# Kernel optimization log

Hardware: AMD Instinct MI355X
Metric: run time of the kernel (lower is better)

## Reference

```python
import jax, jax.numpy as jnp
import numpy as np

K, N, M = 65536, 4096, 64  # observations, basis centers, features


def setup_inputs() -> dict:
    key = jax.random.key(0)
    k1, k2, k3, k4 = jax.random.split(key, 4)
    x = jax.random.normal(k1, (K, M), dtype=jnp.float32)
    x_basis = jax.random.normal(k2, (N, M), dtype=jnp.float32)
    w = jax.random.normal(k3, (1, N), dtype=jnp.float32) / np.sqrt(N)
    b = jax.random.normal(k4, (1,), dtype=jnp.float32)
    return {"x": x, "x_basis": x_basis, "w": w, "b": b}


def reference(x, x_basis, w, b):
    # pairwise squared distances ||x_i - c_j||^2, [K, N]
    x2 = jnp.sum(x * x, axis=1, keepdims=True)          # [K, 1]
    c2 = jnp.sum(x_basis * x_basis, axis=1)             # [N]
    sq = x2 + c2[None, :] - 2.0 * (x @ x_basis.T)       # [K, N]
    phi = jnp.exp(-sq)                                  # gaussian RBF
    return jax.nn.sigmoid(phi @ w.T + b)                # [K, 1]
```

## Files before the change

kernel.cpp:

```cpp
#include <hip/hip_runtime.h>


#define KOBS 65536
#define NCENT 4096
#define MFEAT 64
#define NCHUNK 32

#define SCALE_A 2.8853900817779268f
#define QS      1.4426950408889634f
#define TSKIP   -60.0f

typedef __attribute__((ext_vector_type(4)))  float float4v;
typedef __attribute__((ext_vector_type(2)))  float float2v;
typedef __attribute__((ext_vector_type(16))) float float16v;
typedef __attribute__((ext_vector_type(8)))  int   int8v;

#if __has_builtin(__builtin_amdgcn_exp2f)
#define EXP2F(x) __builtin_amdgcn_exp2f(x)
#else
#define EXP2F(x) exp2f(x)
#endif

#define MFMA(A, B, C) __builtin_amdgcn_mfma_scale_f32_32x32x64_f8f6f4( \
    (A), (B), (C), 0, 0, 0, 0x7f7f7f7f, 0, 0x7f7f7f7f)

__global__ __launch_bounds__(256) void rbf_prep(
    const float* __restrict__ xb, const float* __restrict__ w,
    char* __restrict__ cb, float2v* __restrict__ hc2w) {
    const int bid = blockIdx.x;
    const int tid = threadIdx.x;
    if (bid < 128) {
        const int o      = bid * 256 + tid;
        const int col    = o >> 3;
        const int joct   = o & 7;
        const int c      = col >> 7;
        const int w4     = (col >> 5) & 3;
        const int lanelo = col & 31;
        const int l      = lanelo + (joct >> 2) * 32;
        const int j0     = (joct & 3) * 8;
        const float* src = xb + col * MFEAT + joct * 8;
        float4v v0 = *(const float4v*)(src);
        float4v v1 = *(const float4v*)(src + 4);
        int lo = __builtin_amdgcn_cvt_pk_fp8_f32(v0[0], v0[1], 0, false);
        lo     = __builtin_amdgcn_cvt_pk_fp8_f32(v0[2], v0[3], lo, true);
        int hi = __builtin_amdgcn_cvt_pk_fp8_f32(v1[0], v1[1], 0, false);
        hi     = __builtin_amdgcn_cvt_pk_fp8_f32(v1[2], v1[3], hi, true);
        unsigned long long pk = (unsigned long long)(unsigned)lo |
                                ((unsigned long long)(unsigned)hi << 32);
        *(unsigned long long*)(cb + (size_t)((c * 4 + w4) * 64 + l) * 32 + j0) = pk;
    } else {
        const int row  = (bid - 128) * 4 + (tid >> 6);
        const int lane = tid & 63;
        float v = xb[row * MFEAT + lane];
        float s = v * v;
        #pragma unroll
        for (int off = 32; off > 0; off >>= 1) s += __shfl_xor(s, off, 64);
        if (lane == 0) {
            float2v hw = {TSKIP + QS * s, w[row]};
            hc2w[row] = hw;
        }
    }
}

__global__ __launch_bounds__(512, 4) void rbf_main(
    const float* __restrict__ x, const char* __restrict__ cb,
    const float2v* __restrict__ hc2w, const float* __restrict__ bptr,
    float* __restrict__ out) {
    __shared__ float x2s[128];
    __shared__ float zl[128];

    const int tid  = threadIdx.x;
    const int wv   = tid >> 6;
    const int lane = tid & 63;
    const int ll   = lane & 31;
    const int lh   = lane >> 5;
    const int rt   = wv >> 2;
    const int wq   = wv & 3;
    const int bid  = (int)blockIdx.x;

    if (tid < 128) zl[tid] = 0.0f;

    const int r0e = bid * 128 + rt * 64;
    int8v af0, af1;
    #pragma unroll
    for (int t = 0; t < 2; ++t) {
        const float* xr = x + (size_t)(r0e + t * 32 + ll) * MFEAT + lh * 32;
        int8v a;
        float ss = 0.0f;
        #pragma unroll
        for (int rg = 0; rg < 8; ++rg) {
            float4v v = *(const float4v*)(xr + rg * 4);
            ss = fmaf(v[0], v[0], ss); ss = fmaf(v[1], v[1], ss);
            ss = fmaf(v[2], v[2], ss); ss = fmaf(v[3], v[3], ss);
            int pk = __builtin_amdgcn_cvt_pk_fp8_f32(
                SCALE_A * v[0], SCALE_A * v[1], 0, false);
            pk = __builtin_amdgcn_cvt_pk_fp8_f32(
                SCALE_A * v[2], SCALE_A * v[3], pk, true);
            a[rg] = pk;
        }
        ss += __shfl_xor(ss, 32, 64);
        if (t == 0) af0 = a; else af1 = a;
        if (wq == 0 && lh == 0) x2s[rt * 64 + t * 32 + ll] = ss;
    }
    __syncthreads();

    const int rb = 4 * lh;
    float16v p0, p1;
    #pragma unroll
    for (int i = 0; i < 16; ++i) {
        const int ri = rb + (i & 3) + 8 * (i >> 2);
        p0[i] = -QS * x2s[rt * 64 + ri];
        p1[i] = -QS * x2s[rt * 64 + 32 + ri];
    }

    const int zbase = rt * 64 + rb;
    const char*    cbb = cb + (size_t)(wq * 64 + lane) * 32;
    const float2v* hwp = hc2w + wq * 32 + ll;

    int8v   pb[2];
    float2v phw[2];

    #define LOADB(c, s) do {                                   \
        pb[s]  = *(const int8v*)(cbb + (size_t)(c) * 8192);    \
        phw[s] = hwp[(c) * 128];                               \
    } while (0)

    LOADB(0, 0);

    #pragma unroll 2
    for (int c = 0; c < NCHUNK; ++c) {
        const int cur = c & 1, nxt = cur ^ 1;
        if (c + 1 < NCHUNK) LOADB(c + 1, nxt);
        float16v a0 = MFMA(af0, pb[cur], p0);
        float16v a1 = MFMA(af1, pb[cur], p1);
        const float tq  = phw[cur].x;
        const float wv_ = phw[cur].y;
        #pragma unroll
        for (int t = 0; t < 2; ++t) {
            float16v av = t ? a1 : a0;
            float m0 = fmaxf(fmaxf(av[0],  av[1]),  av[2]);
            float m1 = fmaxf(fmaxf(av[3],  av[4]),  av[5]);
            float m2 = fmaxf(fmaxf(av[6],  av[7]),  av[8]);
            float m3 = fmaxf(fmaxf(av[9],  av[10]), av[11]);
            float m4 = fmaxf(fmaxf(av[12], av[13]), av[14]);
            float mx = fmaxf(fmaxf(fmaxf(m0, m1), m2),
                             fmaxf(fmaxf(m3, m4), av[15]));
            if (__any(mx > tq)) {
                if (mx > tq) {
                    const float q = TSKIP - tq;
                    #pragma unroll
                    for (int i = 0; i < 16; ++i)
                        atomicAdd(&zl[zbase + t * 32 + (i & 3) + 8 * (i >> 2)],
                                  wv_ * EXP2F(av[i] + q));
                }
            }
        }
    }
    #undef LOADB

    __syncthreads();
    if (tid < 128) {
        const float z = zl[tid] + bptr[0];
        out[bid * 128 + tid] = 1.0f / (1.0f + EXP2F(-QS * z));
    }
}

extern "C" void kernel_launch(void* const* d_in, const int* in_sizes, int n_in,
                              void* d_out, int out_size, void* d_ws, size_t ws_size,
                              hipStream_t stream) {
    const float* x  = (const float*)d_in[0];
    const float* xb = (const float*)d_in[1];
    const float* w  = (const float*)d_in[2];
    const float* b  = (const float*)d_in[3];
    float* out = (float*)d_out;

    char*    cb   = (char*)d_ws;
    float2v* hc2w = (float2v*)((char*)d_ws + NCENT * MFEAT);

    rbf_prep<<<128 + NCENT / 4, 256, 0, stream>>>(xb, w, cb, hc2w);
    rbf_main<<<KOBS / 128, 512, 0, stream>>>(x, cb, hc2w, b, out);
}
```

Baseline: 91.09 us.

## Triple-buffer center loads, pack threshold/weight as bf16 pair, merge skip test

Prefetch depth goes from two to three slots, with the chunk loop manually unrolled by three and the last two steps peeled, so B-fragment loads have more time to land before the MFMAs need them. The per-center threshold and weight are packed as two bf16 halves in one 32-bit word instead of a float2, halving that load. The two row-tile skip checks are merged into a single wave vote. The bf16 rounding of the threshold and weight loses precision, which can shift which terms are skipped and slightly change the output.

Result: faster. 88.23 us (-3.1%).

```diff
diff --git a/kernel.cpp b/kernel.cpp
--- a/kernel.cpp
+++ b/kernel.cpp
@@ -11,7 +11,6 @@
 #define TSKIP   -60.0f
 
 typedef __attribute__((ext_vector_type(4)))  float float4v;
-typedef __attribute__((ext_vector_type(2)))  float float2v;
 typedef __attribute__((ext_vector_type(16))) float float16v;
 typedef __attribute__((ext_vector_type(8)))  int   int8v;
 
@@ -21,12 +20,17 @@
 #define EXP2F(x) exp2f(x)
 #endif
 
+static __device__ inline unsigned f2bfu(float f) {
+    unsigned u = __float_as_uint(f);
+    return (u + 0x7fffu + ((u >> 16) & 1u)) >> 16;
+}
+
 #define MFMA(A, B, C) __builtin_amdgcn_mfma_scale_f32_32x32x64_f8f6f4( \
     (A), (B), (C), 0, 0, 0, 0x7f7f7f7f, 0, 0x7f7f7f7f)
 
 __global__ __launch_bounds__(256) void rbf_prep(
     const float* __restrict__ xb, const float* __restrict__ w,
-    char* __restrict__ cb, float2v* __restrict__ hc2w) {
+    char* __restrict__ cb, unsigned* __restrict__ hcw) {
     const int bid = blockIdx.x;
     const int tid = threadIdx.x;
     if (bid < 128) {
@@ -55,16 +59,14 @@
         float s = v * v;
         #pragma unroll
         for (int off = 32; off > 0; off >>= 1) s += __shfl_xor(s, off, 64);
-        if (lane == 0) {
-            float2v hw = {TSKIP + QS * s, w[row]};
-            hc2w[row] = hw;
-        }
+        if (lane == 0)
+            hcw[row] = (f2bfu(TSKIP + QS * s) << 16) | f2bfu(w[row]);
     }
 }
 
 __global__ __launch_bounds__(512, 4) void rbf_main(
     const float* __restrict__ x, const char* __restrict__ cb,
-    const float2v* __restrict__ hc2w, const float* __restrict__ bptr,
+    const unsigned* __restrict__ hcw, const float* __restrict__ bptr,
     float* __restrict__ out) {
     __shared__ float x2s[128];
     __shared__ float zl[128];
@@ -114,48 +116,68 @@
     }
 
     const int zbase = rt * 64 + rb;
-    const char*    cbb = cb + (size_t)(wq * 64 + lane) * 32;
-    const float2v* hwp = hc2w + wq * 32 + ll;
-
-    int8v   pb[2];
-    float2v phw[2];
-
-    #define LOADB(c, s) do {                                   \
-        pb[s]  = *(const int8v*)(cbb + (size_t)(c) * 8192);    \
-        phw[s] = hwp[(c) * 128];                               \
+    const unsigned cboff = (unsigned)(wq * 64 + lane) * 32u;
+    const unsigned moff  = (unsigned)(wq * 32 + ll);
+
+    int8v    pb[3];
+    unsigned mw[3];
+
+    #define LOADB(C, S) do {                                               \
+        pb[S] = *(const int8v*)(cb + cboff + (unsigned)(C) * 8192u);       \
+        mw[S] = hcw[moff + (unsigned)(C) * 128u];                          \
     } while (0)
 
+    #define STEP(C, SCUR, SPRE, DOLOAD) do {                               \
+        if (DOLOAD) LOADB((C) + 2, SPRE);                                  \
+        float16v a0 = MFMA(af0, pb[SCUR], p0);                             \
+        float16v a1 = MFMA(af1, pb[SCUR], p1);                             \
+        const unsigned mu = mw[SCUR];                                      \
+        const float tq  = __uint_as_float(mu & 0xffff0000u);               \
+        const float wv_ = __uint_as_float(mu << 16);                       \
+        float uA0 = fmaxf(fmaxf(a0[0],  a0[1]),  a0[2]);                   \
+        float uA1 = fmaxf(fmaxf(a0[3],  a0[4]),  a0[5]);                   \
+        float uA2 = fmaxf(fmaxf(a0[6],  a0[7]),  a0[8]);                   \
+        float uA3 = fmaxf(fmaxf(a0[9],  a0[10]), a0[11]);                  \
+        float uA4 = fmaxf(fmaxf(a0[12], a0[13]), a0[14]);                  \
+        float mA  = fmaxf(fmaxf(fmaxf(uA0, uA1), uA2),                     \
+                          fmaxf(fmaxf(uA3, uA4), a0[15]));                 \
+        float uB0 = fmaxf(fmaxf(a1[0],  a1[1]),  a1[2]);                   \
+        float uB1 = fmaxf(fmaxf(a1[3],  a1[4]),  a1[5]);                   \
+        float uB2 = fmaxf(fmaxf(a1[6],  a1[7]),  a1[8]);                   \
+        float uB3 = fmaxf(fmaxf(a1[9],  a1[10]), a1[11]);                  \
+        float uB4 = fmaxf(fmaxf(a1[12], a1[13]), a1[14]);                  \
+        float mB  = fmaxf(fmaxf(fmaxf(uB0, uB1), uB2),                     \
+                          fmaxf(fmaxf(uB3, uB4), a1[15]));                 \
+        if (__any(fmaxf(mA, mB) > tq)) {         \
+            const float q = TSKIP - tq;              \
+            if (mA > tq) {                                                 \
+                _Pragma("unroll")                                          \
+                for (int i_ = 0; i_ < 16; ++i_)                            \
+                    atomicAdd(&zl[zbase + (i_ & 3) + 8 * (i_ >> 2)],       \
+                              wv_ * EXP2F(a0[i_] + q));                    \
+            }                                                              \
+            if (mB > tq) {                                                 \
+                _Pragma("unroll")                                          \
+                for (int i_ = 0; i_ < 16; ++i_)                            \
+                    atomicAdd(&zl[zbase + 32 + (i_ & 3) + 8 * (i_ >> 2)],  \
+                              wv_ * EXP2F(a1[i_] + q));                    \
+            }                                                              \
+        }                                                                  \
+    } while (0)
+
     LOADB(0, 0);
-
-    #pragma unroll 2
-    for (int c = 0; c < NCHUNK; ++c) {
-        const int cur = c & 1, nxt = cur ^ 1;
-        if (c + 1 < NCHUNK) LOADB(c + 1, nxt);
-        float16v a0 = MFMA(af0, pb[cur], p0);
-        float16v a1 = MFMA(af1, pb[cur], p1);
-        const float tq  = phw[cur].x;
-        const float wv_ = phw[cur].y;
-        #pragma unroll
-        for (int t = 0; t < 2; ++t) {
-            float16v av = t ? a1 : a0;
-            float m0 = fmaxf(fmaxf(av[0],  av[1]),  av[2]);
-            float m1 = fmaxf(fmaxf(av[3],  av[4]),  av[5]);
-            float m2 = fmaxf(fmaxf(av[6],  av[7]),  av[8]);
-            float m3 = fmaxf(fmaxf(av[9],  av[10]), av[11]);
-            float m4 = fmaxf(fmaxf(av[12], av[13]), av[14]);
-            float mx = fmaxf(fmaxf(fmaxf(m0, m1), m2),
-                             fmaxf(fmaxf(m3, m4), av[15]));
-            if (__any(mx > tq)) {
-                if (mx > tq) {
-                    const float q = TSKIP - tq;
-                    #pragma unroll
-                    for (int i = 0; i < 16; ++i)
-                        atomicAdd(&zl[zbase + t * 32 + (i & 3) + 8 * (i >> 2)],
-                                  wv_ * EXP2F(av[i] + q));
-                }
-            }
-        }
-    }
+    LOADB(1, 1);
+
+    #pragma unroll 1
+    for (int c = 0; c < 30; c += 3) {
+        STEP(c,     0, 2, 1);
+        STEP(c + 1, 1, 0, 1);
+        STEP(c + 2, 2, 1, 1);
+    }
+    STEP(30, 0, 2, 0);
+    STEP(31, 1, 0, 0);
+
+    #undef STEP
     #undef LOADB
 
     __syncthreads();
@@ -174,9 +196,9 @@
     const float* b  = (const float*)d_in[3];
     float* out = (float*)d_out;
 
-    char*    cb   = (char*)d_ws;
-    float2v* hc2w = (float2v*)((char*)d_ws + NCENT * MFEAT);
-
-    rbf_prep<<<128 + NCENT / 4, 256, 0, stream>>>(xb, w, cb, hc2w);
-    rbf_main<<<KOBS / 128, 512, 0, stream>>>(x, cb, hc2w, b, out);
-}
+    char*     cb  = (char*)d_ws;
+    unsigned* hcw = (unsigned*)((char*)d_ws + NCENT * MFEAT);
+
+    rbf_prep<<<128 + NCENT / 4, 256, 0, stream>>>(xb, w, cb, hcw);
+    rbf_main<<<KOBS / 128, 512, 0, stream>>>(x, cb, hcw, b, out);
+}
```

## Stage basis chunks through double-buffered LDS and pack threshold/weight as bf16 pair

Applied to the files above, without the earlier changes.

Each wave used to load its fp8 basis fragment straight from global memory. Now the block cooperatively copies each 8KB chunk into a padded, double-buffered shared-memory tile and syncs once per chunk. This cuts redundant global and L2 traffic, since the two row-tile waves shared the same B data. The per-center threshold and weight are packed as two bf16 values in one 32-bit word, and the skip test is merged across both row tiles. The costs are a block-wide barrier every iteration, no loop unrolling, and reduced precision on the threshold and weight.

Measured after the change: 89.06 us. 1.02x faster.

```diff
diff --git a/kernel.cpp b/kernel.cpp
--- a/kernel.cpp
+++ b/kernel.cpp
@@ -10,10 +10,10 @@
 #define QS      1.4426950408889634f
 #define TSKIP   -60.0f
 
-typedef __attribute__((ext_vector_type(4)))  float float4v;
-typedef __attribute__((ext_vector_type(2)))  float float2v;
-typedef __attribute__((ext_vector_type(16))) float float16v;
-typedef __attribute__((ext_vector_type(8)))  int   int8v;
+typedef __attribute__((ext_vector_type(4)))  float    float4v;
+typedef __attribute__((ext_vector_type(16))) float    float16v;
+typedef __attribute__((ext_vector_type(8)))  int      int8v;
+typedef __attribute__((ext_vector_type(4)))  unsigned uint4v;
 
 #if __has_builtin(__builtin_amdgcn_exp2f)
 #define EXP2F(x) __builtin_amdgcn_exp2f(x)
@@ -21,12 +21,20 @@
 #define EXP2F(x) exp2f(x)
 #endif
 
+static __device__ inline unsigned f2bfu(float f) {
+    unsigned u = __float_as_uint(f);
+    return (u + 0x7fffu + ((u >> 16) & 1u)) >> 16;
+}
+
 #define MFMA(A, B, C) __builtin_amdgcn_mfma_scale_f32_32x32x64_f8f6f4( \
     (A), (B), (C), 0, 0, 0, 0x7f7f7f7f, 0, 0x7f7f7f7f)
 
+#define LROW(r) (((r) >> 2) * 144 + ((r) & 3) * 32)
+#define LBUFSZ  (64 * 144)
+
 __global__ __launch_bounds__(256) void rbf_prep(
     const float* __restrict__ xb, const float* __restrict__ w,
-    char* __restrict__ cb, float2v* __restrict__ hc2w) {
+    char* __restrict__ cb, unsigned* __restrict__ hcw) {
     const int bid = blockIdx.x;
     const int tid = threadIdx.x;
     if (bid < 128) {
@@ -55,19 +63,18 @@
         float s = v * v;
         #pragma unroll
         for (int off = 32; off > 0; off >>= 1) s += __shfl_xor(s, off, 64);
-        if (lane == 0) {
-            float2v hw = {TSKIP + QS * s, w[row]};
-            hc2w[row] = hw;
-        }
+        if (lane == 0)
+            hcw[row] = (f2bfu(TSKIP + QS * s) << 16) | f2bfu(w[row]);
     }
 }
 
 __global__ __launch_bounds__(512, 4) void rbf_main(
     const float* __restrict__ x, const char* __restrict__ cb,
-    const float2v* __restrict__ hc2w, const float* __restrict__ bptr,
+    const unsigned* __restrict__ hcw, const float* __restrict__ bptr,
     float* __restrict__ out) {
     __shared__ float x2s[128];
     __shared__ float zl[128];
+    __shared__ char  bs[2][LBUFSZ];
 
     const int tid  = threadIdx.x;
     const int wv   = tid >> 6;
@@ -102,6 +109,12 @@
         if (t == 0) af0 = a; else af1 = a;
         if (wq == 0 && lh == 0) x2s[rt * 64 + t * 32 + ll] = ss;
     }
+
+    const unsigned sdst = (unsigned)(LROW(tid >> 1) + (tid & 1) * 16);
+    uint4v stg = *(const uint4v*)(cb + tid * 16);
+    unsigned mw = hcw[wq * 32 + ll];
+    *(uint4v*)(bs[0] + sdst) = stg;
+
     __syncthreads();
 
     const int rb = 4 * lh;
@@ -114,51 +127,65 @@
     }
 
     const int zbase = rt * 64 + rb;
-    const char*    cbb = cb + (size_t)(wq * 64 + lane) * 32;
-    const float2v* hwp = hc2w + wq * 32 + ll;
-
-    int8v   pb[2];
-    float2v phw[2];
-
-    #define LOADB(c, s) do {                                   \
-        pb[s]  = *(const int8v*)(cbb + (size_t)(c) * 8192);    \
-        phw[s] = hwp[(c) * 128];                               \
-    } while (0)
-
-    LOADB(0, 0);
-
-    #pragma unroll 2
+    const unsigned moff  = (unsigned)(wq * 32 + ll);
+    const unsigned rdoff = (unsigned)LROW(wq * 64 + lane);
+
+    #pragma unroll 1
     for (int c = 0; c < NCHUNK; ++c) {
-        const int cur = c & 1, nxt = cur ^ 1;
-        if (c + 1 < NCHUNK) LOADB(c + 1, nxt);
-        float16v a0 = MFMA(af0, pb[cur], p0);
-        float16v a1 = MFMA(af1, pb[cur], p1);
-        const float tq  = phw[cur].x;
-        const float wv_ = phw[cur].y;
-        #pragma unroll
-        for (int t = 0; t < 2; ++t) {
-            float16v av = t ? a1 : a0;
-            float m0 = fmaxf(fmaxf(av[0],  av[1]),  av[2]);
-            float m1 = fmaxf(fmaxf(av[3],  av[4]),  av[5]);
-            float m2 = fmaxf(fmaxf(av[6],  av[7]),  av[8]);
-            float m3 = fmaxf(fmaxf(av[9],  av[10]), av[11]);
-            float m4 = fmaxf(fmaxf(av[12], av[13]), av[14]);
-            float mx = fmaxf(fmaxf(fmaxf(m0, m1), m2),
-                             fmaxf(fmaxf(m3, m4), av[15]));
-            if (__any(mx > tq)) {
-                if (mx > tq) {
-                    const float q = TSKIP - tq;
-                    #pragma unroll
-                    for (int i = 0; i < 16; ++i)
-                        atomicAdd(&zl[zbase + t * 32 + (i & 3) + 8 * (i >> 2)],
-                                  wv_ * EXP2F(av[i] + q));
-                }
+        unsigned mwn = mw;
+        if (c + 1 < NCHUNK) {
+            stg = *(const uint4v*)(cb + (size_t)(c + 1) * 8192 + tid * 16);
+            mwn = hcw[moff + (unsigned)(c + 1) * 128u];
+        }
+        const char* lb = bs[c & 1];
+        uint4v blo = *(const uint4v*)(lb + rdoff);
+        uint4v bhi = *(const uint4v*)(lb + rdoff + 16);
+        int8v b;
+        b[0] = (int)blo[0]; b[1] = (int)blo[1]; b[2] = (int)blo[2]; b[3] = (int)blo[3];
+        b[4] = (int)bhi[0]; b[5] = (int)bhi[1]; b[6] = (int)bhi[2]; b[7] = (int)bhi[3];
+
+        float16v a0 = MFMA(af0, b, p0);
+        float16v a1 = MFMA(af1, b, p1);
+
+        const float tq  = __uint_as_float(mw & 0xffff0000u);
+        const float wv_ = __uint_as_float(mw << 16);
+        float uA0 = fmaxf(fmaxf(a0[0],  a0[1]),  a0[2]);
+        float uA1 = fmaxf(fmaxf(a0[3],  a0[4]),  a0[5]);
+        float uA2 = fmaxf(fmaxf(a0[6],  a0[7]),  a0[8]);
+        float uA3 = fmaxf(fmaxf(a0[9],  a0[10]), a0[11]);
+        float uA4 = fmaxf(fmaxf(a0[12], a0[13]), a0[14]);
+        float mA  = fmaxf(fmaxf(fmaxf(uA0, uA1), uA2),
+                          fmaxf(fmaxf(uA3, uA4), a0[15]));
+        float uB0 = fmaxf(fmaxf(a1[0],  a1[1]),  a1[2]);
+        float uB1 = fmaxf(fmaxf(a1[3],  a1[4]),  a1[5]);
+        float uB2 = fmaxf(fmaxf(a1[6],  a1[7]),  a1[8]);
+        float uB3 = fmaxf(fmaxf(a1[9],  a1[10]), a1[11]);
+        float uB4 = fmaxf(fmaxf(a1[12], a1[13]), a1[14]);
+        float mB  = fmaxf(fmaxf(fmaxf(uB0, uB1), uB2),
+                          fmaxf(fmaxf(uB3, uB4), a1[15]));
+        if (__any(fmaxf(mA, mB) > tq)) {
+            const float q = TSKIP - tq;
+            if (mA > tq) {
+                #pragma unroll
+                for (int i_ = 0; i_ < 16; ++i_)
+                    atomicAdd(&zl[zbase + (i_ & 3) + 8 * (i_ >> 2)],
+                              wv_ * EXP2F(a0[i_] + q));
             }
-        }
-    }
-    #undef LOADB
-
-    __syncthreads();
+            if (mB > tq) {
+                #pragma unroll
+                for (int i_ = 0; i_ < 16; ++i_)
+                    atomicAdd(&zl[zbase + 32 + (i_ & 3) + 8 * (i_ >> 2)],
+                              wv_ * EXP2F(a1[i_] + q));
+            }
+        }
+
+        if (c + 1 < NCHUNK) {
+            *(uint4v*)(bs[(c + 1) & 1] + sdst) = stg;
+        }
+        mw = mwn;
+        __syncthreads();
+    }
+
     if (tid < 128) {
         const float z = zl[tid] + bptr[0];
         out[bid * 128 + tid] = 1.0f / (1.0f + EXP2F(-QS * z));
@@ -174,9 +201,9 @@
     const float* b  = (const float*)d_in[3];
     float* out = (float*)d_out;
 
-    char*    cb   = (char*)d_ws;
-    float2v* hc2w = (float2v*)((char*)d_ws + NCENT * MFEAT);
-
-    rbf_prep<<<128 + NCENT / 4, 256, 0, stream>>>(xb, w, cb, hc2w);
-    rbf_main<<<KOBS / 128, 512, 0, stream>>>(x, cb, hc2w, b, out);
-}
+    char*     cb  = (char*)d_ws;
+    unsigned* hcw = (unsigned*)((char*)d_ws + NCENT * MFEAT);
+
+    rbf_prep<<<128 + NCENT / 4, 256, 0, stream>>>(xb, w, cb, hcw);
+    rbf_main<<<KOBS / 128, 512, 0, stream>>>(x, cb, hcw, b, out);
+}
```
